# Kernel tuning notes

Measured on AMD Instinct MI355X. Metric: run time of the kernel, lower is better.

## Reference

```python
import jax, jax.numpy as jnp
import numpy as np

GAMMA = 0.01
INFER_STEP = 4


def softor(xs, axis, gamma=GAMMA):
    # gamma-scaled log-sum-exp 'soft OR', normalized if it exceeds 1 (alphaILP semantics)
    ls = gamma * jax.nn.logsumexp(xs / gamma, axis=axis)
    return ls / jnp.maximum(jnp.max(ls), 1.0)


def _clauses(x, I):
    # x: [B, G] valuations; I: [C, G, S, L] int indices into G.
    # scan over clauses to avoid materializing [C, B, G, S, L]
    def body(_, Ii):
        g = jnp.take(x, Ii, axis=1)                 # [B, G, S, L] gather
        c = softor(jnp.prod(g, axis=-1), axis=-1)   # prod over body literals, soft-OR over substitutions -> [B, G]
        return None, c
    _, Cs = jax.lax.scan(body, None, I)
    return Cs  # [C, B, G]


def _r(x, W, I):
    Cs = _clauses(x, I)                      # [C, B, G]
    Ws = jax.nn.softmax(W, axis=1)           # [m, C]
    H = jnp.einsum('mc,cbg->mbg', Ws, Cs)    # [m, B, G]
    return softor(H, axis=0)                 # [B, G]


def setup_inputs() -> dict:
    key = jax.random.key(0)
    k1, k2, k3 = jax.random.split(key, 3)
    B, G, C, S, L, m = 64, 4096, 32, 16, 4, 1
    x = jax.random.uniform(k1, (B, G), dtype=jnp.float32)       # valuation in [0,1]
    W = jax.random.uniform(k2, (m, C), dtype=jnp.float32)       # clause weights (train=True)
    I = jax.random.randint(k3, (C, G, S, L), 0, G)               # clause index tensor
    return {"x": x, "W": W, "I": I}


def reference(x, W, I):
    R = x
    for _ in range(INFER_STEP):
        # softor over stacked [prev, new] along dim 1 -> [B, 2, G] reduced over axis 1
        R = softor(jnp.stack([R, _r(R, W, I)], axis=1), axis=1)
    return R
```

## Files before the change

### kernel.cpp

```cpp
#include <hip/hip_runtime.h>
#include <hip/hip_fp16.h>

#define Bv 64
#define Gv 4096
#define Cv 32
#define Sv 16
#define NSTEP 4
#define LOG2E 1.4426950408889634f
#define LN2   0.6931471805599453f
#define GAMMA 0.01f
#define RLOG2E_G 144.26950408889634f
#define SHIFT    72.0f
#define UNSHIFT  0.4990659758388636f

#define EXP2R(x) __builtin_amdgcn_exp2f(x)
#define LOG2R(x) __builtin_amdgcn_logf(x)

struct __align__(16) h8 { __half2 h[4]; };
struct __align__(16) f8 { float4 a, b; };

__device__ __forceinline__ float wave_max(float v) {
#pragma unroll
    for (int off = 32; off > 0; off >>= 1)
        v = fmaxf(v, __shfl_xor(v, off, 64));
    return v;
}

__global__ __launch_bounds__(256) void k_itrans(const int4* __restrict__ I4,
                                                uint2* __restrict__ IT) {
    __shared__ int4 lds[64 * 17];
    int blk = blockIdx.x;
    int c = blk >> 6, gc = blk & 63;
    size_t base = ((size_t)c * Gv + gc * 64) * Sv;
#pragma unroll
    for (int i = 0; i < 4; ++i) {
        int e = threadIdx.x + i * 256;
        int4 ii = I4[base + e];
        lds[(e >> 4) * 17 + (e & 15)] = ii;
    }
    __syncthreads();
    size_t obase = (size_t)(c * 64 + gc) * 1024;
#pragma unroll
    for (int i = 0; i < 4; ++i) {
        int o = threadIdx.x + i * 256;
        int4 ii = lds[(o & 63) * 17 + (o >> 6)];
        uint2 p;
        p.x = ((unsigned)ii.x << 4) | ((unsigned)ii.y << 20);
        p.y = ((unsigned)ii.z << 4) | ((unsigned)ii.w << 20);
        IT[obase + o] = p;
    }
}

__global__ __launch_bounds__(256) void k_transpose(const float* __restrict__ x,
                                                   f8* __restrict__ L8) {
    __shared__ float tile[64][65];
    int g0 = blockIdx.x * 64;
#pragma unroll
    for (int i = 0; i < 16; ++i) {
        int t = threadIdx.x + i * 256;
        int b = t >> 6, gi = t & 63;
        tile[gi][b] = x[b * Gv + g0 + gi];
    }
    __syncthreads();
#pragma unroll
    for (int e = 0; e < 2; ++e) {
        int idx = threadIdx.x + e * 256;
        int gi = idx & 63, oct = idx >> 6;
        f8 fv;
        fv.a = make_float4(tile[gi][oct * 8 + 0], tile[gi][oct * 8 + 1],
                           tile[gi][oct * 8 + 2], tile[gi][oct * 8 + 3]);
        fv.b = make_float4(tile[gi][oct * 8 + 4], tile[gi][oct * 8 + 5],
                           tile[gi][oct * 8 + 6], tile[gi][oct * 8 + 7]);
        L8[oct * Gv + g0 + gi] = fv;
    }
}

__global__ __attribute__((amdgpu_flat_work_group_size(1024, 1024),
                          amdgpu_waves_per_eu(8, 8)))
void k_clauses(const f8* __restrict__ Lprev, const float* __restrict__ LmPrev,
               const uint2* __restrict__ IT, h8* __restrict__ Csh8,
               float* __restrict__ Mc) {
    __shared__ h8 tbl[Gv];
    __shared__ float smax[16];
    int tid = threadIdx.x;
    int blk = blockIdx.x;
    int c    = blk >> 4;
    int oct  = (blk >> 1) & 7;
    int ghalf = blk & 1;

    float rd = 1.0f / fmaxf(LmPrev[0], 1.0f);
    const f8* __restrict__ src = Lprev + (size_t)oct * Gv;
#pragma unroll
    for (int i = 0; i < 4; ++i) {
        f8 v = src[tid + i * 1024];
        h8 hv;
        hv.h[0] = __floats2half2_rn(v.a.x * rd, v.a.y * rd);
        hv.h[1] = __floats2half2_rn(v.a.z * rd, v.a.w * rd);
        hv.h[2] = __floats2half2_rn(v.b.x * rd, v.b.y * rd);
        hv.h[3] = __floats2half2_rn(v.b.z * rd, v.b.w * rd);
        tbl[tid + i * 1024] = hv;
    }
    __syncthreads();

    int lane = tid & 63, wid = tid >> 6;
    const char* tb = (const char*)tbl;
    float vmax = 0.0f;

#pragma unroll
    for (int iter = 0; iter < 2; ++iter) {
        int gc = ghalf * 32 + wid * 2 + iter;
        const uint2* __restrict__ Ig = IT + (size_t)(c * 64 + gc) * 1024 + lane;

        float sum[8];
#pragma unroll
        for (int e = 0; e < 8; ++e) sum[e] = 0.0f;

#pragma unroll
        for (int s = 0; s < Sv; ++s) {
            uint2 u = Ig[s * 64];
            unsigned a0 = u.x & 0xFFFFu, a1 = u.x >> 16;
            unsigned a2 = u.y & 0xFFFFu, a3 = u.y >> 16;
            h8 A = *(const h8*)(tb + a0);
            h8 B = *(const h8*)(tb + a1);
            h8 E = *(const h8*)(tb + a2);
            h8 D = *(const h8*)(tb + a3);
#pragma unroll
            for (int j = 0; j < 4; ++j) {
                __half2 q = __hmul2(__hmul2(A.h[j], B.h[j]), __hmul2(E.h[j], D.h[j]));
                sum[2 * j]     += EXP2R(fmaf(__low2float(q),  RLOG2E_G, -SHIFT));
                sum[2 * j + 1] += EXP2R(fmaf(__high2float(q), RLOG2E_G, -SHIFT));
            }
        }

        float ls[8];
#pragma unroll
        for (int e = 0; e < 8; ++e)
            ls[e] = fmaf(GAMMA * LN2, LOG2R(sum[e]), UNSHIFT);

        h8 outv;
#pragma unroll
        for (int j = 0; j < 4; ++j)
            outv.h[j] = __floats2half2_rn(ls[2 * j], ls[2 * j + 1]);
        Csh8[((size_t)c * 8 + oct) * Gv + gc * 64 + lane] = outv;

#pragma unroll
        for (int e = 0; e < 8; ++e) vmax = fmaxf(vmax, ls[e]);
    }

    vmax = wave_max(vmax);
    if (lane == 0) smax[wid] = vmax;
    __syncthreads();
    if (tid == 0) {
        float m = smax[0];
#pragma unroll
        for (int i = 1; i < 16; ++i) m = fmaxf(m, smax[i]);
        atomicMax((int*)(Mc + c), __float_as_int(m));
    }
}

__global__ __launch_bounds__(256) void k_combupd(const h8* __restrict__ Csh8,
                                                 const float* __restrict__ W,
                                                 const float* __restrict__ Mc,
                                                 const f8* __restrict__ Lprev,
                                                 const float* __restrict__ LmPrev,
                                                 f8* __restrict__ Lout,
                                                 float* __restrict__ LmOut) {
    __shared__ float smax[4];
    __shared__ float scoef[Cv];
    if (threadIdx.x < Cv) {
        int c = threadIdx.x;
        float e = EXP2R(W[c] * LOG2E);
        float wsum = e;
#pragma unroll
        for (int off = 16; off > 0; off >>= 1)
            wsum += __shfl_xor(wsum, off, 64);
        scoef[c] = e / (wsum * fmaxf(Mc[c], 1.0f));
    }
    __syncthreads();

    int tid = blockIdx.x * 256 + threadIdx.x;
    float h[8];
#pragma unroll
    for (int e = 0; e < 8; ++e) h[e] = 0.0f;
#pragma unroll
    for (int c = 0; c < Cv; ++c) {
        float w = scoef[c];
        h8 v = Csh8[(size_t)c * (Gv * 8) + tid];
#pragma unroll
        for (int j = 0; j < 4; ++j) {
            h[2 * j]     = fmaf(w, __low2float(v.h[j]),  h[2 * j]);
            h[2 * j + 1] = fmaf(w, __high2float(v.h[j]), h[2 * j + 1]);
        }
    }

    float rd = 1.0f / fmaxf(LmPrev[0], 1.0f);
    f8 r = Lprev[tid];
    const float* rp = &r.a.x;
    f8 outv;
    float* op = &outv.a.x;
    float vmax = 0.0f;
#pragma unroll
    for (int e = 0; e < 8; ++e) {
        float hn = h[e];
        float rv = rp[e] * rd;
        float mx = fmaxf(rv, hn), mn = fminf(rv, hn);
        float t  = EXP2R((mn - mx) * RLOG2E_G);
        float ls = fmaf(GAMMA * LN2, LOG2R(1.0f + t), mx);
        op[e] = ls;
        vmax = fmaxf(vmax, ls);
    }
    Lout[tid] = outv;
    vmax = wave_max(vmax);
    int lane = threadIdx.x & 63, wid = threadIdx.x >> 6;
    if (lane == 0) smax[wid] = vmax;
    __syncthreads();
    if (threadIdx.x == 0) {
        float m = fmaxf(fmaxf(smax[0], smax[1]), fmaxf(smax[2], smax[3]));
        atomicMax((int*)LmOut, __float_as_int(m));
    }
}

__global__ __launch_bounds__(256) void k_out(const float4* __restrict__ Lraw4,
                                             const float* __restrict__ Lm,
                                             float* __restrict__ out) {
    int tid = blockIdx.x * 256 + threadIdx.x;
    float d = fmaxf(Lm[0], 1.0f);
    float4 lv = Lraw4[tid];
    int lin = tid * 4;
    int oct = lin >> 15;
    int g   = (lin >> 3) & (Gv - 1);
    int k0  = lin & 7;
    int b   = oct * 8 + k0;
    out[(b + 0) * Gv + g] = lv.x / d;
    out[(b + 1) * Gv + g] = lv.y / d;
    out[(b + 2) * Gv + g] = lv.z / d;
    out[(b + 3) * Gv + g] = lv.w / d;
}

extern "C" void kernel_launch(void* const* d_in, const int* in_sizes, int n_in,
                              void* d_out, int out_size, void* d_ws, size_t ws_size,
                              hipStream_t stream) {
    const float* x = (const float*)d_in[0];
    const float* W = (const float*)d_in[1];
    const int*   I = (const int*)d_in[2];
    float* out = (float*)d_out;

    float*  ws    = (float*)d_ws;
    f8*     LrawA = (f8*)ws;
    f8*     LrawB = (f8*)(ws + 262144);
    float*  maxb  = ws + 524288;
    __half* Csh   = (__half*)(ws + 1048576);
    uint2*  ITp   = (uint2*) (ws + 5242880);

    (void)hipMemsetAsync(maxb, 0, (NSTEP * 64 + 64) * sizeof(float), stream);
    k_itrans   <<<Cv * 64, 256, 0, stream>>>((const int4*)I, ITp);
    k_transpose<<<Gv / 64, 256, 0, stream>>>(x, LrawA);

    const float* LmPrev = maxb + NSTEP * 64;
    f8* prev = LrawA;
    f8* cur  = LrawB;
    for (int step = 0; step < NSTEP; ++step) {
        float* Mc = maxb + step * 64;
        float* Lm = Mc + 32;
        k_clauses<<<512, 1024, 0, stream>>>(prev, LmPrev, (const uint2*)ITp,
                                            (h8*)Csh, Mc);
        k_combupd<<<(Bv * Gv) / 2048, 256, 0, stream>>>((const h8*)Csh, W, Mc,
                                                        prev, LmPrev, cur, Lm);
        LmPrev = Lm;
        f8* t = prev; prev = cur; cur = t;
    }
    k_out<<<(Bv * Gv) / 1024, 256, 0, stream>>>((const float4*)prev, LmPrev, out);
}
```

Baseline: 171.5 us.

## Gather fourth clause literal from a global half-precision copy instead of LDS

```diff
diff --git a/kernel.cpp b/kernel.cpp
--- a/kernel.cpp
+++ b/kernel.cpp
@@ -52,7 +52,8 @@
 }
 
 __global__ __launch_bounds__(256) void k_transpose(const float* __restrict__ x,
-                                                   f8* __restrict__ L8) {
+                                                   f8* __restrict__ L8,
+                                                   h8* __restrict__ LH) {
     __shared__ float tile[64][65];
     int g0 = blockIdx.x * 64;
 #pragma unroll
@@ -72,14 +73,20 @@
         fv.b = make_float4(tile[gi][oct * 8 + 4], tile[gi][oct * 8 + 5],
                            tile[gi][oct * 8 + 6], tile[gi][oct * 8 + 7]);
         L8[oct * Gv + g0 + gi] = fv;
+        h8 hv;
+        hv.h[0] = __floats2half2_rn(fv.a.x, fv.a.y);
+        hv.h[1] = __floats2half2_rn(fv.a.z, fv.a.w);
+        hv.h[2] = __floats2half2_rn(fv.b.x, fv.b.y);
+        hv.h[3] = __floats2half2_rn(fv.b.z, fv.b.w);
+        LH[oct * Gv + g0 + gi] = hv;
     }
 }
 
 __global__ __attribute__((amdgpu_flat_work_group_size(1024, 1024),
                           amdgpu_waves_per_eu(8, 8)))
 void k_clauses(const f8* __restrict__ Lprev, const float* __restrict__ LmPrev,
-               const uint2* __restrict__ IT, h8* __restrict__ Csh8,
-               float* __restrict__ Mc) {
+               const h8* __restrict__ LH, const uint2* __restrict__ IT,
+               h8* __restrict__ Csh8, float* __restrict__ Mc) {
     __shared__ h8 tbl[Gv];
     __shared__ float smax[16];
     int tid = threadIdx.x;
@@ -88,8 +95,10 @@
     int oct  = (blk >> 1) & 7;
     int ghalf = blk & 1;
 
-    float rd = 1.0f / fmaxf(LmPrev[0], 1.0f);
+    float rd  = 1.0f / fmaxf(LmPrev[0], 1.0f);
+    float rdk = rd * RLOG2E_G;
     const f8* __restrict__ src = Lprev + (size_t)oct * Gv;
+    const char* __restrict__ LHo = (const char*)(LH + (size_t)oct * Gv);
 #pragma unroll
     for (int i = 0; i < 4; ++i) {
         f8 v = src[tid + i * 1024];
@@ -123,12 +132,12 @@
             h8 A = *(const h8*)(tb + a0);
             h8 B = *(const h8*)(tb + a1);
             h8 E = *(const h8*)(tb + a2);
-            h8 D = *(const h8*)(tb + a3);
+            h8 D = *(const h8*)(LHo + a3);
 #pragma unroll
             for (int j = 0; j < 4; ++j) {
                 __half2 q = __hmul2(__hmul2(A.h[j], B.h[j]), __hmul2(E.h[j], D.h[j]));
-                sum[2 * j]     += EXP2R(fmaf(__low2float(q),  RLOG2E_G, -SHIFT));
-                sum[2 * j + 1] += EXP2R(fmaf(__high2float(q), RLOG2E_G, -SHIFT));
+                sum[2 * j]     += EXP2R(fmaf(__low2float(q),  rdk, -SHIFT));
+                sum[2 * j + 1] += EXP2R(fmaf(__high2float(q), rdk, -SHIFT));
             }
         }
 
@@ -164,6 +173,7 @@
                                                  const f8* __restrict__ Lprev,
                                                  const float* __restrict__ LmPrev,
                                                  f8* __restrict__ Lout,
+                                                 h8* __restrict__ LHout,
                                                  float* __restrict__ LmOut) {
     __shared__ float smax[4];
     __shared__ float scoef[Cv];
@@ -210,6 +220,13 @@
         vmax = fmaxf(vmax, ls);
     }
     Lout[tid] = outv;
+    h8 hv;
+    hv.h[0] = __floats2half2_rn(outv.a.x, outv.a.y);
+    hv.h[1] = __floats2half2_rn(outv.a.z, outv.a.w);
+    hv.h[2] = __floats2half2_rn(outv.b.x, outv.b.y);
+    hv.h[3] = __floats2half2_rn(outv.b.z, outv.b.w);
+    LHout[tid] = hv;
+
     vmax = wave_max(vmax);
     int lane = threadIdx.x & 63, wid = threadIdx.x >> 6;
     if (lane == 0) smax[wid] = vmax;
@@ -249,25 +266,28 @@
     f8*     LrawA = (f8*)ws;
     f8*     LrawB = (f8*)(ws + 262144);
     float*  maxb  = ws + 524288;
+    h8*     LHA   = (h8*)(ws + 655360);
+    h8*     LHB   = (h8*)(ws + 786432);
     __half* Csh   = (__half*)(ws + 1048576);
     uint2*  ITp   = (uint2*) (ws + 5242880);
 
     (void)hipMemsetAsync(maxb, 0, (NSTEP * 64 + 64) * sizeof(float), stream);
     k_itrans   <<<Cv * 64, 256, 0, stream>>>((const int4*)I, ITp);
-    k_transpose<<<Gv / 64, 256, 0, stream>>>(x, LrawA);
+    k_transpose<<<Gv / 64, 256, 0, stream>>>(x, LrawA, LHA);
 
     const float* LmPrev = maxb + NSTEP * 64;
-    f8* prev = LrawA;
-    f8* cur  = LrawB;
+    f8* prev = LrawA;  h8* prevH = LHA;
+    f8* cur  = LrawB;  h8* curH  = LHB;
     for (int step = 0; step < NSTEP; ++step) {
         float* Mc = maxb + step * 64;
         float* Lm = Mc + 32;
-        k_clauses<<<512, 1024, 0, stream>>>(prev, LmPrev, (const uint2*)ITp,
+        k_clauses<<<512, 1024, 0, stream>>>(prev, LmPrev, prevH, (const uint2*)ITp,
                                             (h8*)Csh, Mc);
         k_combupd<<<(Bv * Gv) / 2048, 256, 0, stream>>>((const h8*)Csh, W, Mc,
-                                                        prev, LmPrev, cur, Lm);
+                                                        prev, LmPrev, cur, curH, Lm);
         LmPrev = Lm;
         f8* t = prev; prev = cur; cur = t;
+        h8* th = prevH; prevH = curH; curH = th;
     }
     k_out<<<(Bv * Gv) / 1024, 256, 0, stream>>>((const float4*)prev, LmPrev, out);
 }
```

Result: slower. 266.7 us (+55.5%).
